# Kernel optimization log

Hardware: AMD Instinct MI355X
Metric: run time of the kernel (lower is better)

## Reference

```python
import jax, jax.numpy as jnp
import numpy as np

MAX_BOXES = 50
NOOBJ_SCALE = 1.0
OBJ_SCALE = 5.0
COORD_SCALE = 1.0
CLASS_SCALE = 1.0
SIL_THRESH = 0.6


def setup_inputs() -> dict:
    key = jax.random.key(0)
    k1, k2, k3, k4 = jax.random.split(key, 4)
    nB, nA, nC, nH, nW = 32, 5, 20, 64, 64
    output = jax.random.normal(k1, (nB, nA * (5 + nC), nH, nW), jnp.float32) * 0.5
    # targets: 12 valid boxes per image, rest zero (loop-break semantics)
    K = 12
    cls = jax.random.randint(k2, (nB, MAX_BOXES, 1), 0, nC).astype(jnp.float32)
    xy = jax.random.uniform(k3, (nB, MAX_BOXES, 2), minval=0.05, maxval=0.95)
    wh = jax.random.uniform(k4, (nB, MAX_BOXES, 2), minval=0.05, maxval=0.3)
    boxes = jnp.concatenate([cls, xy, wh], axis=-1)          # [nB, 50, 5]
    valid = (jnp.arange(MAX_BOXES) < K)[None, :, None].astype(jnp.float32)
    target = (boxes * valid).reshape(nB, MAX_BOXES * 5)
    anchors = jnp.array([1.3221, 1.73145, 3.19275, 4.00944, 5.05587,
                         8.09892, 9.47112, 4.84053, 11.2364, 10.0071], jnp.float32)
    return {"output": output, "target": target, "anchors": anchors}


def _iou(b1, b2):
    # center-format boxes (cx, cy, w, h) on the last axis, broadcastable
    l = jnp.maximum(b1[..., 0] - b1[..., 2] * 0.5, b2[..., 0] - b2[..., 2] * 0.5)
    r = jnp.minimum(b1[..., 0] + b1[..., 2] * 0.5, b2[..., 0] + b2[..., 2] * 0.5)
    t = jnp.maximum(b1[..., 1] - b1[..., 3] * 0.5, b2[..., 1] - b2[..., 3] * 0.5)
    b = jnp.minimum(b1[..., 1] + b1[..., 3] * 0.5, b2[..., 1] + b2[..., 3] * 0.5)
    inter = jnp.clip(r - l, 0.0) * jnp.clip(b - t, 0.0)
    union = b1[..., 2] * b1[..., 3] + b2[..., 2] * b2[..., 3] - inter
    return inter / jnp.maximum(union, 1e-10)


def reference(output, target, anchors):
    nB, _, nH, nW = output.shape
    nA = anchors.shape[0] // 2
    nC = output.shape[1] // nA - 5
    out = output.reshape(nB, nA, 5 + nC, nH, nW)

    x = jax.nn.sigmoid(out[:, :, 0])            # [nB,nA,nH,nW]
    y = jax.nn.sigmoid(out[:, :, 1])
    w = out[:, :, 2]
    h = out[:, :, 3]
    conf = jax.nn.sigmoid(out[:, :, 4])
    cls_logits = jnp.transpose(out[:, :, 5:], (0, 1, 3, 4, 2))  # [nB,nA,nH,nW,nC]

    aw = anchors[0::2]
    ah = anchors[1::2]
    grid_x = jnp.arange(nW, dtype=output.dtype)
    grid_y = jnp.arange(nH, dtype=output.dtype)[:, None]
    px = x + grid_x
    py = y + grid_y
    pw = jnp.exp(w) * aw[None, :, None, None]
    ph = jnp.exp(h) * ah[None, :, None, None]
    # build_targets consumes pred_boxes.data -> no grad through it
    pred = jax.lax.stop_gradient(jnp.stack([px, py, pw, ph], axis=-1))  # [nB,nA,nH,nW,4]

    tgt = target.reshape(nB, -1, 5)             # (cls, x, y, w, h)
    T = tgt.shape[1]
    valid = tgt[:, :, 1] > 0
    gx = tgt[:, :, 1] * nW
    gy = tgt[:, :, 2] * nH
    gw = tgt[:, :, 3] * nW
    gh = tgt[:, :, 4] * nH
    gboxes = jnp.stack([gx, gy, gw, gh], axis=-1)  # [nB,T,4]

    # conf_mask: zero out anchors whose IoU with any gt exceeds sil_thresh
    pred_flat = pred.reshape(nB, nA * nH * nW, 4)
    ious = _iou(pred_flat[:, :, None, :], gboxes[:, None, :, :])   # [nB,nAnchors,T]
    max_iou = jnp.max(jnp.where(valid[:, None, :], ious, 0.0), axis=-1)
    conf_base = jnp.where(max_iou.reshape(nB, nA, nH, nW) > SIL_THRESH, 0.0, NOOBJ_SCALE)

    # best anchor per gt: IoU of (0,0,gw,gh) vs (0,0,aw,ah)
    inter_a = jnp.minimum(gw[..., None], aw) * jnp.minimum(gh[..., None], ah)
    iou_a = inter_a / jnp.maximum(gw[..., None] * gh[..., None] + aw * ah - inter_a, 1e-10)
    best_n = jnp.argmax(iou_a, axis=-1)          # [nB,T]

    gi = jnp.clip(jnp.floor(gx), 0, nW - 1).astype(jnp.int32)
    gj = jnp.clip(jnp.floor(gy), 0, nH - 1).astype(jnp.int32)
    bidx = jnp.arange(nB)[:, None]
    N = nB * nA * nH * nW
    flat = ((bidx * nA + best_n) * nH + gj) * nW + gi
    flat = jnp.where(valid, flat, N).reshape(-1)   # invalid gts go to dummy slot N

    def scat(base, vals):
        padded = jnp.concatenate([base.reshape(-1), jnp.zeros((1,), base.dtype)])
        return padded.at[flat].set(vals.reshape(-1))[:N].reshape(nB, nA, nH, nW)

    zeros4 = jnp.zeros((nB, nA, nH, nW), output.dtype)
    half4 = jnp.full((nB, nA, nH, nW), 0.5, output.dtype)
    # seen < 12800 branch: coord_mask all ones, tx=ty=0.5, tw=th=0 as base
    coord_mask = jnp.ones((nB, nA, nH, nW), output.dtype)
    tx = scat(half4, gx - gi.astype(output.dtype))
    ty = scat(half4, gy - gj.astype(output.dtype))
    tw = scat(zeros4, jnp.log(jnp.maximum(gw, 1e-10) / aw[best_n]))
    th = scat(zeros4, jnp.log(jnp.maximum(gh, 1e-10) / ah[best_n]))
    cls_mask = scat(zeros4, jnp.ones((nB, T), output.dtype))
    conf_mask = scat(conf_base, jnp.full((nB, T), OBJ_SCALE, output.dtype))

    pred_pad = jnp.concatenate([pred.reshape(N, 4), jnp.zeros((1, 4), pred.dtype)])
    psel = pred_pad[flat]                         # [nB*T,4]
    iou_gt = _iou(gboxes.reshape(-1, 4), psel)
    tconf = scat(zeros4, iou_gt)
    tcls = scat(zeros4, tgt[:, :, 0])

    tx, ty, tw, th, tconf = map(jax.lax.stop_gradient, (tx, ty, tw, th, tconf))

    cm = coord_mask
    loss_x = COORD_SCALE * 0.5 * jnp.sum((x * cm - tx * cm) ** 2)
    loss_y = COORD_SCALE * 0.5 * jnp.sum((y * cm - ty * cm) ** 2)
    loss_w = COORD_SCALE * 0.5 * jnp.sum((w * cm - tw * cm) ** 2)
    loss_h = COORD_SCALE * 0.5 * jnp.sum((h * cm - th * cm) ** 2)
    sq = jnp.sqrt(conf_mask)
    loss_conf = 0.5 * jnp.sum((conf * sq - tconf * sq) ** 2)
    logp = jax.nn.log_softmax(cls_logits, axis=-1)
    picked = jnp.take_along_axis(logp, tcls.astype(jnp.int32)[..., None], axis=-1)[..., 0]
    loss_cls = CLASS_SCALE * (-(picked * cls_mask).sum())
    return loss_x + loss_y + loss_w + loss_h + loss_conf + loss_cls
```

## Files before the change

### kernel.cpp

```cpp
#include <hip/hip_runtime.h>
#include <math.h>

#define NB 32
#define NA 5
#define NC 20
#define NH 64
#define NW 64
#define MAXB 50
#define CELLS_PER_BLOCK 512
#define BLOCKS_PER_BATCH 40
#define NBLK 1280
#define OBJ_SCALE 5.0f
#define SILC 0.375f

__device__ __forceinline__ float fsig(float v) {
    return __builtin_amdgcn_rcpf(1.0f + __expf(-v));
}

__device__ __forceinline__ float iou_full(float x1, float y1, float w1, float h1,
                                          float x2, float y2, float w2, float h2) {
    float l = fmaxf(x1 - 0.5f * w1, x2 - 0.5f * w2);
    float r = fminf(x1 + 0.5f * w1, x2 + 0.5f * w2);
    float t = fmaxf(y1 - 0.5f * h1, y2 - 0.5f * h2);
    float b = fminf(y1 + 0.5f * h1, y2 + 0.5f * h2);
    float inter = fmaxf(r - l, 0.0f) * fmaxf(b - t, 0.0f);
    float uni = w1 * h1 + w2 * h2 - inter;
    return inter / fmaxf(uni, 1e-10f);
}

__global__ __launch_bounds__(256) void region_main(
        const float* __restrict__ out, const float* __restrict__ target,
        const float* __restrict__ anchors, float* __restrict__ ws) {
    __shared__ float s_t[MAXB * 5];
    __shared__ float s_box[250];
    __shared__ int s_flat[64];
    __shared__ int s_nv;
    __shared__ float s_p[4];

    const int tid = threadIdx.x;
    const int blk = blockIdx.x;
    const int b = blk / BLOCKS_PER_BATCH;
    const int rb = blk - b * BLOCKS_PER_BATCH;

    const int a = rb >> 3;
    const int ji0 = (rb & 7) * CELLS_PER_BLOCK;
    const float* obase = out + ((size_t)(b * 125 + a * 25) << 12);
    const float* b0 = obase + ji0 + tid;
    const float* b1 = b0 + 256;
    float xr0 = b0[0], yr0 = b0[4096], wr0 = b0[2 * 4096], hr0 = b0[3 * 4096], cr0 = b0[4 * 4096];
    float xr1 = b1[0], yr1 = b1[4096], wr1 = b1[2 * 4096], hr1 = b1[3 * 4096], cr1 = b1[4 * 4096];

    const float* tg = target + b * MAXB * 5;
    if (tid < 250) s_t[tid] = tg[tid];
    __syncthreads();

    float v = 0.0f;

    if (tid < 64) {
        bool valid = false;
        float gx = 0, gy = 0, gw = 0, gh = 0, clsf = 0;
        if (tid < MAXB) {
            clsf = s_t[tid * 5 + 0];
            float xx = s_t[tid * 5 + 1];
            gx = xx * 64.0f;
            gy = s_t[tid * 5 + 2] * 64.0f;
            gw = s_t[tid * 5 + 3] * 64.0f;
            gh = s_t[tid * 5 + 4] * 64.0f;
            valid = xx > 0.0f;
        }
        unsigned long long mask = __ballot(valid);
        int pos = __popcll(mask & ((1ull << tid) - 1ull));
        int nv = __popcll(mask);
        if (valid) {
            s_box[pos]       = gx - 0.5f * gw;
            s_box[50 + pos]  = gx + 0.5f * gw;
            s_box[100 + pos] = gy - 0.5f * gh;
            s_box[150 + pos] = gy + 0.5f * gh;
            s_box[200 + pos] = SILC * gw * gh;
        }
        if (tid == 0) s_nv = nv;

        if (rb == 0) {
            float aw_[NA], ah_[NA];
            for (int q = 0; q < NA; ++q) { aw_[q] = anchors[2 * q]; ah_[q] = anchors[2 * q + 1]; }
            int best_n = 0, gi = 0, gj = 0, myflat = -1;
            if (valid) {
                float besti = -1.0f;
                for (int q = 0; q < NA; ++q) {
                    float inter = fminf(gw, aw_[q]) * fminf(gh, ah_[q]);
                    float iou = inter / fmaxf(gw * gh + aw_[q] * ah_[q] - inter, 1e-10f);
                    if (iou > besti) { besti = iou; best_n = q; }
                }
                gi = min(max((int)floorf(gx), 0), 63);
                gj = min(max((int)floorf(gy), 0), 63);
                myflat = (best_n << 12) | (gj << 6) | gi;
            }
            s_flat[tid] = myflat;

            bool winner = (myflat >= 0);
            if (winner) {
                for (int t2 = tid + 1; t2 < MAXB; ++t2)
                    if (s_flat[t2] == myflat) { winner = false; break; }
            }
            if (winner) {
                const float* basep = out + ((size_t)(b * 125 + best_n * 25) << 12)
                                   + (gj << 6) + gi;
                float xr = basep[0];
                float yr = basep[1 * 4096];
                float wr = basep[2 * 4096];
                float hr = basep[3 * 4096];
                float cr = basep[4 * 4096];

                float x = fsig(xr), y = fsig(yr), conf = fsig(cr);
                float aw = aw_[best_n], ah = ah_[best_n];
                float pw = __expf(wr) * aw, ph = __expf(hr) * ah;
                float px = x + (float)gi, py = y + (float)gj;
                float pl = px - 0.5f * pw, pr2 = px + 0.5f * pw;
                float pt = py - 0.5f * ph, pb2 = py + 0.5f * ph;
                float pa375 = SILC * (pw * ph);

                bool hit = false;
                for (int k = 0; k < nv; ++k) {
                    float l = fmaxf(pl, s_box[k]);
                    float r = fminf(pr2, s_box[50 + k]);
                    float t = fmaxf(pt, s_box[100 + k]);
                    float bo = fminf(pb2, s_box[150 + k]);
                    float inter = fmaxf(r - l, 0.0f) * fmaxf(bo - t, 0.0f);
                    hit = hit || (inter > pa375 + s_box[200 + k]);
                }
                float cb = hit ? 0.0f : 1.0f;

                float txv = gx - (float)gi;
                float tyv = gy - (float)gj;
                float twv = __logf(fmaxf(gw, 1e-10f) / aw);
                float thv = __logf(fmaxf(gh, 1e-10f) / ah);
                float tconf = iou_full(gx, gy, gw, gh, px, py, pw, ph);

                float dxn = x - txv, dyn = y - tyv, dwn = wr - twv, dhn = hr - thv;
                float dxo = x - 0.5f, dyo = y - 0.5f;
                float dc = conf - tconf;

                v += 0.5f * ((dxn * dxn - dxo * dxo) + (dyn * dyn - dyo * dyo)
                           + (dwn * dwn - wr * wr) + (dhn * dhn - hr * hr))
                   + 0.5f * (OBJ_SCALE * dc * dc - cb * conf * conf);

                const float* cl = basep + 5 * 4096;
                float lg[NC];
                float m = -INFINITY;
                for (int c = 0; c < NC; ++c) { lg[c] = cl[c * 4096]; m = fmaxf(m, lg[c]); }
                float s = 0.0f;
                for (int c = 0; c < NC; ++c) s += __expf(lg[c] - m);
                int ci = (int)clsf;
                v -= (lg[ci] - m - __logf(s));
            }
        }
    }
    __syncthreads();

    const float aw = anchors[2 * a], ah = anchors[2 * a + 1];
    const int nv = s_nv;

    int cell0 = ji0 + tid;
    int i0 = cell0 & 63, j0 = (cell0 >> 6) & 63;
    int cell1 = cell0 + 256;
    int i1 = cell1 & 63, j1 = (cell1 >> 6) & 63;

    float x0 = fsig(xr0), y0 = fsig(yr0), c0 = fsig(cr0);
    float x1 = fsig(xr1), y1 = fsig(yr1), c1 = fsig(cr1);
    float pw0 = __expf(wr0) * aw, ph0 = __expf(hr0) * ah;
    float pw1 = __expf(wr1) * aw, ph1 = __expf(hr1) * ah;
    float px0 = x0 + (float)i0, py0 = y0 + (float)j0;
    float px1 = x1 + (float)i1, py1 = y1 + (float)j1;
    float pl0 = px0 - 0.5f * pw0, pr0 = px0 + 0.5f * pw0;
    float pt0 = py0 - 0.5f * ph0, pb0 = py0 + 0.5f * ph0;
    float pl1 = px1 - 0.5f * pw1, pr1 = px1 + 0.5f * pw1;
    float pt1 = py1 - 0.5f * ph1, pb1 = py1 + 0.5f * ph1;
    float pa0 = SILC * (pw0 * ph0);
    float pa1 = SILC * (pw1 * ph1);

    bool hit0 = false, hit1 = false;
    for (int k = 0; k < nv; ++k) {
        float bl = s_box[k];
        float br = s_box[50 + k];
        float bt = s_box[100 + k];
        float bb = s_box[150 + k];
        float th = s_box[200 + k];
        float in0 = fmaxf(fminf(pr0, br) - fmaxf(pl0, bl), 0.0f)
                  * fmaxf(fminf(pb0, bb) - fmaxf(pt0, bt), 0.0f);
        float in1 = fmaxf(fminf(pr1, br) - fmaxf(pl1, bl), 0.0f)
                  * fmaxf(fminf(pb1, bb) - fmaxf(pt1, bt), 0.0f);
        hit0 = hit0 || (in0 > pa0 + th);
        hit1 = hit1 || (in1 > pa1 + th);
    }

    float dx0 = x0 - 0.5f, dy0 = y0 - 0.5f;
    float dx1 = x1 - 0.5f, dy1 = y1 - 0.5f;
    v += 0.5f * (dx0 * dx0 + dy0 * dy0 + wr0 * wr0 + hr0 * hr0)
       + 0.5f * (hit0 ? 0.0f : 1.0f) * c0 * c0
       + 0.5f * (dx1 * dx1 + dy1 * dy1 + wr1 * wr1 + hr1 * hr1)
       + 0.5f * (hit1 ? 0.0f : 1.0f) * c1 * c1;

    for (int off = 32; off; off >>= 1) v += __shfl_down(v, off);
    if ((tid & 63) == 0) s_p[tid >> 6] = v;
    __syncthreads();
    if (tid == 0)
        ws[blk] = s_p[0] + s_p[1] + s_p[2] + s_p[3];
}

__global__ __launch_bounds__(256) void region_reduce(
        const float* __restrict__ ws, float* __restrict__ loss) {
    __shared__ float s_p[4];
    const int tid = threadIdx.x;
    float v = 0.0f;
    for (int idx = tid; idx < NBLK; idx += 256) v += ws[idx];
    for (int off = 32; off; off >>= 1) v += __shfl_down(v, off);
    if ((tid & 63) == 0) s_p[tid >> 6] = v;
    __syncthreads();
    if (tid == 0) loss[0] = s_p[0] + s_p[1] + s_p[2] + s_p[3];
}

extern "C" void kernel_launch(void* const* d_in, const int* in_sizes, int n_in,
                              void* d_out, int out_size, void* d_ws, size_t ws_size,
                              hipStream_t stream) {
    (void)in_sizes; (void)n_in; (void)ws_size; (void)out_size;
    const float* output  = (const float*)d_in[0];
    const float* target  = (const float*)d_in[1];
    const float* anchors = (const float*)d_in[2];
    float* ws = (float*)d_ws;
    float* loss = (float*)d_out;

    region_main<<<NBLK, 256, 0, stream>>>(output, target, anchors, ws);
    region_reduce<<<1, 256, 0, stream>>>(ws, loss);
}
```

Measured before the change: 100.6 us.

## Split per-truth work into separate blocks and double cells per dense thread

The per-ground-truth work (anchor match, dedup, class softmax), which used to run inside the first dense block of each image, moves into 32 dedicated extra blocks so no dense block carries that serial tail. Dense blocks now cover 1024 cells each, four per thread, which halves the block count and amortises the target staging and box setup over more cells. The final reduction drops to a single wavefront. The cost is more registers per thread and fewer blocks to hide memory latency.

```diff
diff --git a/kernel.cpp b/kernel.cpp
--- a/kernel.cpp
+++ b/kernel.cpp
@@ -4,12 +4,12 @@
 #define NB 32
 #define NA 5
 #define NC 20
-#define NH 64
-#define NW 64
 #define MAXB 50
-#define CELLS_PER_BLOCK 512
-#define BLOCKS_PER_BATCH 40
-#define NBLK 1280
+#define CELLS_PER_BLOCK 1024
+#define BLOCKS_PER_BATCH 20
+#define NBLK_DENSE 640
+#define NBLK_TOTAL (NBLK_DENSE + NB)
+#define NPART NBLK_TOTAL
 #define OBJ_SCALE 5.0f
 #define SILC 0.375f
 
@@ -39,24 +39,14 @@
 
     const int tid = threadIdx.x;
     const int blk = blockIdx.x;
-    const int b = blk / BLOCKS_PER_BATCH;
-    const int rb = blk - b * BLOCKS_PER_BATCH;
-
-    const int a = rb >> 3;
-    const int ji0 = (rb & 7) * CELLS_PER_BLOCK;
-    const float* obase = out + ((size_t)(b * 125 + a * 25) << 12);
-    const float* b0 = obase + ji0 + tid;
-    const float* b1 = b0 + 256;
-    float xr0 = b0[0], yr0 = b0[4096], wr0 = b0[2 * 4096], hr0 = b0[3 * 4096], cr0 = b0[4 * 4096];
-    float xr1 = b1[0], yr1 = b1[4096], wr1 = b1[2 * 4096], hr1 = b1[3 * 4096], cr1 = b1[4 * 4096];
-
-    const float* tg = target + b * MAXB * 5;
-    if (tid < 250) s_t[tid] = tg[tid];
-    __syncthreads();
-
-    float v = 0.0f;
-
-    if (tid < 64) {
+
+    if (blk >= NBLK_DENSE) {
+        const int b = blk - NBLK_DENSE;
+        const float* tg = target + b * MAXB * 5;
+        if (tid < 250) s_t[tid] = tg[tid];
+        __syncthreads();
+        if (tid >= 64) return;
+
         bool valid = false;
         float gx = 0, gy = 0, gw = 0, gh = 0, clsf = 0;
         if (tid < MAXB) {
@@ -78,127 +68,185 @@
             s_box[150 + pos] = gy + 0.5f * gh;
             s_box[200 + pos] = SILC * gw * gh;
         }
-        if (tid == 0) s_nv = nv;
-
-        if (rb == 0) {
-            float aw_[NA], ah_[NA];
-            for (int q = 0; q < NA; ++q) { aw_[q] = anchors[2 * q]; ah_[q] = anchors[2 * q + 1]; }
-            int best_n = 0, gi = 0, gj = 0, myflat = -1;
-            if (valid) {
-                float besti = -1.0f;
-                for (int q = 0; q < NA; ++q) {
-                    float inter = fminf(gw, aw_[q]) * fminf(gh, ah_[q]);
-                    float iou = inter / fmaxf(gw * gh + aw_[q] * ah_[q] - inter, 1e-10f);
-                    if (iou > besti) { besti = iou; best_n = q; }
-                }
-                gi = min(max((int)floorf(gx), 0), 63);
-                gj = min(max((int)floorf(gy), 0), 63);
-                myflat = (best_n << 12) | (gj << 6) | gi;
+
+        float aw_[NA], ah_[NA];
+        for (int q = 0; q < NA; ++q) { aw_[q] = anchors[2 * q]; ah_[q] = anchors[2 * q + 1]; }
+        int best_n = 0, gi = 0, gj = 0, myflat = -1;
+        if (valid) {
+            float besti = -1.0f;
+            for (int q = 0; q < NA; ++q) {
+                float inter = fminf(gw, aw_[q]) * fminf(gh, ah_[q]);
+                float iou = inter / fmaxf(gw * gh + aw_[q] * ah_[q] - inter, 1e-10f);
+                if (iou > besti) { besti = iou; best_n = q; }
             }
-            s_flat[tid] = myflat;
-
-            bool winner = (myflat >= 0);
-            if (winner) {
-                for (int t2 = tid + 1; t2 < MAXB; ++t2)
-                    if (s_flat[t2] == myflat) { winner = false; break; }
+            gi = min(max((int)floorf(gx), 0), 63);
+            gj = min(max((int)floorf(gy), 0), 63);
+            myflat = (best_n << 12) | (gj << 6) | gi;
+        }
+        s_flat[tid] = myflat;
+
+        bool winner = (myflat >= 0);
+        if (winner) {
+            for (int t2 = tid + 1; t2 < MAXB; ++t2)
+                if (s_flat[t2] == myflat) { winner = false; break; }
+        }
+
+        float v = 0.0f;
+        if (winner) {
+            const float* basep = out + ((size_t)(b * 125 + best_n * 25) << 12)
+                               + (gj << 6) + gi;
+            float xr = basep[0];
+            float yr = basep[1 * 4096];
+            float wr = basep[2 * 4096];
+            float hr = basep[3 * 4096];
+            float cr = basep[4 * 4096];
+
+            float x = fsig(xr), y = fsig(yr), conf = fsig(cr);
+            float aw = aw_[best_n], ah = ah_[best_n];
+            float pw = __expf(wr) * aw, ph = __expf(hr) * ah;
+            float px = x + (float)gi, py = y + (float)gj;
+            float pl = px - 0.5f * pw, pr2 = px + 0.5f * pw;
+            float pt = py - 0.5f * ph, pb2 = py + 0.5f * ph;
+            float pa375 = SILC * (pw * ph);
+
+            bool hit = false;
+            for (int k = 0; k < nv; ++k) {
+                float l = fmaxf(pl, s_box[k]);
+                float r = fminf(pr2, s_box[50 + k]);
+                float t = fmaxf(pt, s_box[100 + k]);
+                float bo = fminf(pb2, s_box[150 + k]);
+                float inter = fmaxf(r - l, 0.0f) * fmaxf(bo - t, 0.0f);
+                hit = hit || (inter > pa375 + s_box[200 + k]);
             }
-            if (winner) {
-                const float* basep = out + ((size_t)(b * 125 + best_n * 25) << 12)
-                                   + (gj << 6) + gi;
-                float xr = basep[0];
-                float yr = basep[1 * 4096];
-                float wr = basep[2 * 4096];
-                float hr = basep[3 * 4096];
-                float cr = basep[4 * 4096];
-
-                float x = fsig(xr), y = fsig(yr), conf = fsig(cr);
-                float aw = aw_[best_n], ah = ah_[best_n];
-                float pw = __expf(wr) * aw, ph = __expf(hr) * ah;
-                float px = x + (float)gi, py = y + (float)gj;
-                float pl = px - 0.5f * pw, pr2 = px + 0.5f * pw;
-                float pt = py - 0.5f * ph, pb2 = py + 0.5f * ph;
-                float pa375 = SILC * (pw * ph);
-
-                bool hit = false;
-                for (int k = 0; k < nv; ++k) {
-                    float l = fmaxf(pl, s_box[k]);
-                    float r = fminf(pr2, s_box[50 + k]);
-                    float t = fmaxf(pt, s_box[100 + k]);
-                    float bo = fminf(pb2, s_box[150 + k]);
-                    float inter = fmaxf(r - l, 0.0f) * fmaxf(bo - t, 0.0f);
-                    hit = hit || (inter > pa375 + s_box[200 + k]);
-                }
-                float cb = hit ? 0.0f : 1.0f;
-
-                float txv = gx - (float)gi;
-                float tyv = gy - (float)gj;
-                float twv = __logf(fmaxf(gw, 1e-10f) / aw);
-                float thv = __logf(fmaxf(gh, 1e-10f) / ah);
-                float tconf = iou_full(gx, gy, gw, gh, px, py, pw, ph);
-
-                float dxn = x - txv, dyn = y - tyv, dwn = wr - twv, dhn = hr - thv;
-                float dxo = x - 0.5f, dyo = y - 0.5f;
-                float dc = conf - tconf;
-
-                v += 0.5f * ((dxn * dxn - dxo * dxo) + (dyn * dyn - dyo * dyo)
-                           + (dwn * dwn - wr * wr) + (dhn * dhn - hr * hr))
-                   + 0.5f * (OBJ_SCALE * dc * dc - cb * conf * conf);
-
-                const float* cl = basep + 5 * 4096;
-                float lg[NC];
-                float m = -INFINITY;
-                for (int c = 0; c < NC; ++c) { lg[c] = cl[c * 4096]; m = fmaxf(m, lg[c]); }
-                float s = 0.0f;
-                for (int c = 0; c < NC; ++c) s += __expf(lg[c] - m);
-                int ci = (int)clsf;
-                v -= (lg[ci] - m - __logf(s));
-            }
-        }
+            float cb = hit ? 0.0f : 1.0f;
+
+            float txv = gx - (float)gi;
+            float tyv = gy - (float)gj;
+            float twv = __logf(fmaxf(gw, 1e-10f) / aw);
+            float thv = __logf(fmaxf(gh, 1e-10f) / ah);
+            float tconf = iou_full(gx, gy, gw, gh, px, py, pw, ph);
+
+            float dxn = x - txv, dyn = y - tyv, dwn = wr - twv, dhn = hr - thv;
+            float dxo = x - 0.5f, dyo = y - 0.5f;
+            float dc = conf - tconf;
+
+            v = 0.5f * ((dxn * dxn - dxo * dxo) + (dyn * dyn - dyo * dyo)
+                      + (dwn * dwn - wr * wr) + (dhn * dhn - hr * hr))
+              + 0.5f * (OBJ_SCALE * dc * dc - cb * conf * conf);
+
+            const float* cl = basep + 5 * 4096;
+            float lg[NC];
+            float m = -INFINITY;
+            for (int c = 0; c < NC; ++c) { lg[c] = cl[c * 4096]; m = fmaxf(m, lg[c]); }
+            float s = 0.0f;
+            for (int c = 0; c < NC; ++c) s += __expf(lg[c] - m);
+            int ci = (int)clsf;
+            v -= (lg[ci] - m - __logf(s));
+        }
+
+        for (int off = 32; off; off >>= 1) v += __shfl_down(v, off);
+        if (tid == 0) ws[NBLK_DENSE + b] = v;
+        return;
+    }
+
+    const int b = blk / BLOCKS_PER_BATCH;
+    const int rb = blk - b * BLOCKS_PER_BATCH;
+    const int a = rb >> 2;
+    const int ji0 = (rb & 3) * CELLS_PER_BLOCK;
+    const float* obase = out + ((size_t)(b * 125 + a * 25) << 12);
+
+    const float* b0 = obase + ji0 + tid;
+    float xr0 = b0[0],        yr0 = b0[4096],        wr0 = b0[2*4096],        hr0 = b0[3*4096],        cr0 = b0[4*4096];
+    float xr1 = b0[256],      yr1 = b0[4096+256],    wr1 = b0[2*4096+256],    hr1 = b0[3*4096+256],    cr1 = b0[4*4096+256];
+    float xr2 = b0[512],      yr2 = b0[4096+512],    wr2 = b0[2*4096+512],    hr2 = b0[3*4096+512],    cr2 = b0[4*4096+512];
+    float xr3 = b0[768],      yr3 = b0[4096+768],    wr3 = b0[2*4096+768],    hr3 = b0[3*4096+768],    cr3 = b0[4*4096+768];
+
+    const float* tg = target + b * MAXB * 5;
+    if (tid < 250) s_t[tid] = tg[tid];
+    __syncthreads();
+
+    if (tid < 64) {
+        bool valid = false;
+        float gx = 0, gy = 0, gw = 0, gh = 0;
+        if (tid < MAXB) {
+            float xx = s_t[tid * 5 + 1];
+            gx = xx * 64.0f;
+            gy = s_t[tid * 5 + 2] * 64.0f;
+            gw = s_t[tid * 5 + 3] * 64.0f;
+            gh = s_t[tid * 5 + 4] * 64.0f;
+            valid = xx > 0.0f;
+        }
+        unsigned long long mask = __ballot(valid);
+        int pos = __popcll(mask & ((1ull << tid) - 1ull));
+        if (valid) {
+            s_box[pos]       = gx - 0.5f * gw;
+            s_box[50 + pos]  = gx + 0.5f * gw;
+            s_box[100 + pos] = gy - 0.5f * gh;
+            s_box[150 + pos] = gy + 0.5f * gh;
+            s_box[200 + pos] = SILC * gw * gh;
+        }
+        if (tid == 0) s_nv = __popcll(mask);
     }
     __syncthreads();
 
     const float aw = anchors[2 * a], ah = anchors[2 * a + 1];
     const int nv = s_nv;
 
-    int cell0 = ji0 + tid;
-    int i0 = cell0 & 63, j0 = (cell0 >> 6) & 63;
-    int cell1 = cell0 + 256;
-    int i1 = cell1 & 63, j1 = (cell1 >> 6) & 63;
-
-    float x0 = fsig(xr0), y0 = fsig(yr0), c0 = fsig(cr0);
-    float x1 = fsig(xr1), y1 = fsig(yr1), c1 = fsig(cr1);
+    const int c0 = ji0 + tid;
+    const float i0 = (float)(c0 & 63),         j0 = (float)((c0 >> 6) & 63);
+    const float i1 = (float)((c0+256) & 63),   j1 = (float)(((c0+256) >> 6) & 63);
+    const float i2 = (float)((c0+512) & 63),   j2 = (float)(((c0+512) >> 6) & 63);
+    const float i3 = (float)((c0+768) & 63),   j3 = (float)(((c0+768) >> 6) & 63);
+
+    float x0 = fsig(xr0), y0 = fsig(yr0), cf0 = fsig(cr0);
+    float x1 = fsig(xr1), y1 = fsig(yr1), cf1 = fsig(cr1);
+    float x2 = fsig(xr2), y2 = fsig(yr2), cf2 = fsig(cr2);
+    float x3 = fsig(xr3), y3 = fsig(yr3), cf3 = fsig(cr3);
     float pw0 = __expf(wr0) * aw, ph0 = __expf(hr0) * ah;
     float pw1 = __expf(wr1) * aw, ph1 = __expf(hr1) * ah;
-    float px0 = x0 + (float)i0, py0 = y0 + (float)j0;
-    float px1 = x1 + (float)i1, py1 = y1 + (float)j1;
-    float pl0 = px0 - 0.5f * pw0, pr0 = px0 + 0.5f * pw0;
-    float pt0 = py0 - 0.5f * ph0, pb0 = py0 + 0.5f * ph0;
-    float pl1 = px1 - 0.5f * pw1, pr1 = px1 + 0.5f * pw1;
-    float pt1 = py1 - 0.5f * ph1, pb1 = py1 + 0.5f * ph1;
+    float pw2 = __expf(wr2) * aw, ph2 = __expf(hr2) * ah;
+    float pw3 = __expf(wr3) * aw, ph3 = __expf(hr3) * ah;
+
+    float pl0 = x0 + i0 - 0.5f*pw0, pr0 = x0 + i0 + 0.5f*pw0;
+    float pt0 = y0 + j0 - 0.5f*ph0, pb0 = y0 + j0 + 0.5f*ph0;
+    float pl1 = x1 + i1 - 0.5f*pw1, pr1 = x1 + i1 + 0.5f*pw1;
+    float pt1 = y1 + j1 - 0.5f*ph1, pb1 = y1 + j1 + 0.5f*ph1;
+    float pl2 = x2 + i2 - 0.5f*pw2, pr2 = x2 + i2 + 0.5f*pw2;
+    float pt2 = y2 + j2 - 0.5f*ph2, pb2 = y2 + j2 + 0.5f*ph2;
+    float pl3 = x3 + i3 - 0.5f*pw3, pr3 = x3 + i3 + 0.5f*pw3;
+    float pt3 = y3 + j3 - 0.5f*ph3, pb3 = y3 + j3 + 0.5f*ph3;
     float pa0 = SILC * (pw0 * ph0);
     float pa1 = SILC * (pw1 * ph1);
-
-    bool hit0 = false, hit1 = false;
+    float pa2 = SILC * (pw2 * ph2);
+    float pa3 = SILC * (pw3 * ph3);
+
+    bool h0 = false, h1 = false, h2 = false, h3 = false;
     for (int k = 0; k < nv; ++k) {
         float bl = s_box[k];
         float br = s_box[50 + k];
         float bt = s_box[100 + k];
         float bb = s_box[150 + k];
         float th = s_box[200 + k];
-        float in0 = fmaxf(fminf(pr0, br) - fmaxf(pl0, bl), 0.0f)
-                  * fmaxf(fminf(pb0, bb) - fmaxf(pt0, bt), 0.0f);
-        float in1 = fmaxf(fminf(pr1, br) - fmaxf(pl1, bl), 0.0f)
-                  * fmaxf(fminf(pb1, bb) - fmaxf(pt1, bt), 0.0f);
-        hit0 = hit0 || (in0 > pa0 + th);
-        hit1 = hit1 || (in1 > pa1 + th);
+        float n0 = fmaxf(fminf(pr0, br) - fmaxf(pl0, bl), 0.0f) * fmaxf(fminf(pb0, bb) - fmaxf(pt0, bt), 0.0f);
+        float n1 = fmaxf(fminf(pr1, br) - fmaxf(pl1, bl), 0.0f) * fmaxf(fminf(pb1, bb) - fmaxf(pt1, bt), 0.0f);
+        float n2 = fmaxf(fminf(pr2, br) - fmaxf(pl2, bl), 0.0f) * fmaxf(fminf(pb2, bb) - fmaxf(pt2, bt), 0.0f);
+        float n3 = fmaxf(fminf(pr3, br) - fmaxf(pl3, bl), 0.0f) * fmaxf(fminf(pb3, bb) - fmaxf(pt3, bt), 0.0f);
+        h0 = h0 || (n0 > pa0 + th);
+        h1 = h1 || (n1 > pa1 + th);
+        h2 = h2 || (n2 > pa2 + th);
+        h3 = h3 || (n3 > pa3 + th);
     }
 
-    float dx0 = x0 - 0.5f, dy0 = y0 - 0.5f;
-    float dx1 = x1 - 0.5f, dy1 = y1 - 0.5f;
-    v += 0.5f * (dx0 * dx0 + dy0 * dy0 + wr0 * wr0 + hr0 * hr0)
-       + 0.5f * (hit0 ? 0.0f : 1.0f) * c0 * c0
-       + 0.5f * (dx1 * dx1 + dy1 * dy1 + wr1 * wr1 + hr1 * hr1)
-       + 0.5f * (hit1 ? 0.0f : 1.0f) * c1 * c1;
+    float dx, dy;
+    float v = 0.0f;
+    dx = x0 - 0.5f; dy = y0 - 0.5f;
+    v += 0.5f * (dx*dx + dy*dy + wr0*wr0 + hr0*hr0) + 0.5f * (h0 ? 0.0f : 1.0f) * cf0 * cf0;
+    dx = x1 - 0.5f; dy = y1 - 0.5f;
+    v += 0.5f * (dx*dx + dy*dy + wr1*wr1 + hr1*hr1) + 0.5f * (h1 ? 0.0f : 1.0f) * cf1 * cf1;
+    dx = x2 - 0.5f; dy = y2 - 0.5f;
+    v += 0.5f * (dx*dx + dy*dy + wr2*wr2 + hr2*hr2) + 0.5f * (h2 ? 0.0f : 1.0f) * cf2 * cf2;
+    dx = x3 - 0.5f; dy = y3 - 0.5f;
+    v += 0.5f * (dx*dx + dy*dy + wr3*wr3 + hr3*hr3) + 0.5f * (h3 ? 0.0f : 1.0f) * cf3 * cf3;
 
     for (int off = 32; off; off >>= 1) v += __shfl_down(v, off);
     if ((tid & 63) == 0) s_p[tid >> 6] = v;
@@ -207,16 +255,13 @@
         ws[blk] = s_p[0] + s_p[1] + s_p[2] + s_p[3];
 }
 
-__global__ __launch_bounds__(256) void region_reduce(
+__global__ __launch_bounds__(64) void region_reduce(
         const float* __restrict__ ws, float* __restrict__ loss) {
-    __shared__ float s_p[4];
     const int tid = threadIdx.x;
     float v = 0.0f;
-    for (int idx = tid; idx < NBLK; idx += 256) v += ws[idx];
+    for (int idx = tid; idx < NPART; idx += 64) v += ws[idx];
     for (int off = 32; off; off >>= 1) v += __shfl_down(v, off);
-    if ((tid & 63) == 0) s_p[tid >> 6] = v;
-    __syncthreads();
-    if (tid == 0) loss[0] = s_p[0] + s_p[1] + s_p[2] + s_p[3];
+    if (tid == 0) loss[0] = v;
 }
 
 extern "C" void kernel_launch(void* const* d_in, const int* in_sizes, int n_in,
@@ -229,6 +274,6 @@
     float* ws = (float*)d_ws;
     float* loss = (float*)d_out;
 
-    region_main<<<NBLK, 256, 0, stream>>>(output, target, anchors, ws);
-    region_reduce<<<1, 256, 0, stream>>>(ws, loss);
-}
+    region_main<<<NBLK_TOTAL, 256, 0, stream>>>(output, target, anchors, ws);
+    region_reduce<<<1, 64, 0, stream>>>(ws, loss);
+}
```

Result: no change. 101.8 us (+1.2%).
